# Performance work log

Measured on AMD Instinct MI355X. Metric: run time of the kernel, lower is better.

## Reference

```python
import jax, jax.numpy as jnp
import numpy as np

NUM_STUDENTS = 50000
NUM_PROBLEMS = 10000
EMBED_DIM = 64
NNZ = 3200000


def _spmm(rows, cols, vals, x, num_out):
    # out[r] = sum_{edges e with rows[e]==r} vals[e] * x[cols[e]]
    msgs = vals[:, None] * x[cols]  # [nnz, d]
    return jax.ops.segment_sum(msgs, rows, num_segments=num_out)


def setup_inputs() -> dict:
    key = jax.random.key(0)
    ks = jax.random.split(key, 8)
    return {
        "student_embeds": jax.random.normal(ks[0], (NUM_STUDENTS, EMBED_DIM), jnp.float32),
        "problem_embeds": jax.random.normal(ks[1], (NUM_PROBLEMS, EMBED_DIM), jnp.float32),
        "a_rows": jax.random.randint(ks[2], (NNZ,), 0, NUM_STUDENTS, jnp.int32),
        "a_cols": jax.random.randint(ks[3], (NNZ,), 0, NUM_PROBLEMS, jnp.int32),
        "a_vals": jax.random.uniform(ks[4], (NNZ,), jnp.float32),
        "ia_rows": jax.random.randint(ks[5], (NNZ,), 0, NUM_STUDENTS, jnp.int32),
        "ia_cols": jax.random.randint(ks[6], (NNZ,), 0, NUM_PROBLEMS, jnp.int32),
        "ia_vals": jax.random.uniform(ks[7], (NNZ,), jnp.float32),
    }


def reference(student_embeds, problem_embeds, a_rows, a_cols, a_vals,
              ia_rows, ia_cols, ia_vals):
    num_students = student_embeds.shape[0]
    num_problems = problem_embeds.shape[0]
    # a_matrix @ problem_embeds
    student_embeds_c = _spmm(a_rows, a_cols, a_vals, problem_embeds, num_students)
    # a_matrix.T @ student_embeds (swap roles of rows/cols)
    problem_embeds_c = _spmm(a_cols, a_rows, a_vals, student_embeds, num_problems)
    student_embeds_ic = _spmm(ia_rows, ia_cols, ia_vals, problem_embeds, num_students)
    problem_embeds_ic = _spmm(ia_cols, ia_rows, ia_vals, student_embeds, num_problems)
    return (student_embeds_c, student_embeds_ic, problem_embeds_c, problem_embeds_ic)
```

## Files before the change

### kernel.cpp

```cpp
#include <hip/hip_runtime.h>
#include <hip/hip_bf16.h>

#define NBMAX 256
#define TILE  4096
#define KPT   16
#define BINSMAX 512

__device__ __forceinline__ int seg8(unsigned r, unsigned mult8) {
    return (int)__umulhi(r, mult8);
}

__global__ __launch_bounds__(256) void hist_all(
        const int* __restrict__ k0, const int* __restrict__ k1,
        const int* __restrict__ k2, const int* __restrict__ k3,
        int* __restrict__ gcnt4, int nnz, int rsh_s, int rsh_p) {
    __shared__ int h[NBMAX];
    int dir = blockIdx.x & 3;
    const int* key = (dir == 0) ? k0 : (dir == 1) ? k1 : (dir == 2) ? k2 : k3;
    int rsh = (dir & 1) ? rsh_p : rsh_s;
    h[threadIdx.x] = 0;
    __syncthreads();
    int ch = blockIdx.x >> 2, nch = gridDim.x >> 2;
    int nnz4 = nnz >> 2;
    for (int i = ch * 256 + threadIdx.x; i < nnz4; i += nch * 256) {
        int4 k4 = ((const int4*)key)[i];
        atomicAdd(&h[k4.x >> rsh], 1);
        atomicAdd(&h[k4.y >> rsh], 1);
        atomicAdd(&h[k4.z >> rsh], 1);
        atomicAdd(&h[k4.w >> rsh], 1);
    }
    if (ch == 0) {
        for (int i = (nnz4 << 2) + threadIdx.x; i < nnz; i += 256)
            atomicAdd(&h[key[i] >> rsh], 1);
    }
    __syncthreads();
    int v = h[threadIdx.x];
    if (v) atomicAdd(&gcnt4[dir * NBMAX + threadIdx.x], v);
}

__global__ __launch_bounds__(256) void scan_all(
        const int* __restrict__ gcnt4, int* __restrict__ boffs4,
        int* __restrict__ bcur4, int nb_s, int nb_p, int nnz,
        int* __restrict__ offsE, int* __restrict__ offsO, int NS, int NP8) {
    __shared__ int tmp[NBMAX];
    int dir = blockIdx.x, tid = threadIdx.x;
    int nb = (dir & 1) ? nb_p : nb_s;
    int v = (tid < nb) ? gcnt4[dir * NBMAX + tid] : 0;
    tmp[tid] = v;
    __syncthreads();
    for (int off = 1; off < NBMAX; off <<= 1) {
        int t = (tid >= off) ? tmp[tid - off] : 0;
        __syncthreads();
        tmp[tid] += t;
        __syncthreads();
    }
    if (tid < nb) {
        int e = tmp[tid] - v;
        boffs4[dir * (NBMAX + 1) + tid] = e;
        bcur4[dir * NBMAX + tid] = e;
    }
    if (tid == 0) boffs4[dir * (NBMAX + 1) + nb] = nnz;
    if (dir == 0 && tid == 0) { offsE[NS] = nnz; offsO[NP8] = nnz; }
}

__global__ __launch_bounds__(256) void staged_scatter(
        const int* __restrict__ key, const int* __restrict__ other,
        const float* __restrict__ vals, int* __restrict__ cursor,
        uint2* __restrict__ edges, int nnz, int rsh) {
    __shared__ int lhist[NBMAX], lofs[NBMAX], lbase[NBMAX];
    __shared__ uint2 stage[TILE];
    __shared__ int   sslot[TILE];
    int tid = threadIdx.x;
    int lmask = (1 << rsh) - 1;
    int ntiles = (nnz + TILE - 1) / TILE;
    for (int tile = blockIdx.x; tile < ntiles; tile += gridDim.x) {
        int tbeg = tile * TILE;
        int n = nnz - tbeg; if (n > TILE) n = TILE;
        lhist[tid] = 0;
        __syncthreads();
        int myb[KPT], myr[KPT]; unsigned myo[KPT]; float myv[KPT];
        #pragma unroll
        for (int g = 0; g < 4; ++g) {
            int s = g * 1024 + tid * 4;
            if (s + 4 <= n) {
                int i = tbeg + s;
                int4   k4 = *(const int4*)(key + i);
                int4   o4 = *(const int4*)(other + i);
                float4 v4 = *(const float4*)(vals + i);
                int   kk[4] = {k4.x, k4.y, k4.z, k4.w};
                int   oo[4] = {o4.x, o4.y, o4.z, o4.w};
                float vv[4] = {v4.x, v4.y, v4.z, v4.w};
                #pragma unroll
                for (int k = 0; k < 4; ++k) {
                    int m = g * 4 + k;
                    myb[m] = kk[k] >> rsh;
                    myo[m] = (unsigned)oo[k] | ((unsigned)(kk[k] & lmask) << 16);
                    myv[m] = vv[k];
                    myr[m] = atomicAdd(&lhist[myb[m]], 1);
                }
            } else {
                #pragma unroll
                for (int k = 0; k < 4; ++k) {
                    int m = g * 4 + k;
                    int s2 = s + k;
                    if (s2 < n) {
                        int i = tbeg + s2;
                        int ky = key[i];
                        myb[m] = ky >> rsh;
                        myo[m] = (unsigned)other[i] | ((unsigned)(ky & lmask) << 16);
                        myv[m] = vals[i];
                        myr[m] = atomicAdd(&lhist[myb[m]], 1);
                    } else myb[m] = -1;
                }
            }
        }
        __syncthreads();
        int h = lhist[tid];
        lofs[tid] = h;
        __syncthreads();
        for (int off = 1; off < NBMAX; off <<= 1) {
            int t = (tid >= off) ? lofs[tid - off] : 0;
            __syncthreads();
            lofs[tid] += t;
            __syncthreads();
        }
        lofs[tid] -= h;
        if (h > 0) lbase[tid] = atomicAdd(&cursor[tid], h);
        __syncthreads();
        #pragma unroll
        for (int k = 0; k < KPT; ++k) {
            if (myb[k] >= 0) {
                int ls = lofs[myb[k]] + myr[k];
                stage[ls] = make_uint2(myo[k], __float_as_uint(myv[k]));
                sslot[ls] = lbase[myb[k]] + myr[k];
            }
        }
        __syncthreads();
        #pragma unroll
        for (int k = 0; k < KPT; ++k) {
            int s = k * 256 + tid;
            if (s < n) edges[sslot[s]] = stage[s];
        }
        __syncthreads();
    }
}

__global__ __launch_bounds__(512) void row_sort1(
        const uint2* __restrict__ e1, uint2* __restrict__ e2,
        const int* __restrict__ boffs, int* __restrict__ offs,
        int odd, int nb, int rsh, int nrows, unsigned mult8) {
    __shared__ int cnt[BINSMAX];
    __shared__ int tot[512];
    int tid = threadIdx.x;
    int b = blockIdx.x;
    if (b >= nb) return;
    int bins = odd ? (8 << rsh) : (1 << rsh);
    int beg = boffs[b], end = boffs[b + 1];
    if (tid < bins) cnt[tid] = 0;
    __syncthreads();
    for (int i = beg + tid; i < end; i += 512) {
        uint2 e = e1[i];
        int lrow = (int)(e.x >> 16);
        int bin = odd ? (lrow * 8 + seg8(e.x & 0xFFFFu, mult8)) : lrow;
        atomicAdd(&cnt[bin], 1);
    }
    __syncthreads();
    int own = (tid < bins) ? cnt[tid] : 0;
    tot[tid] = own;
    __syncthreads();
    for (int off = 1; off < 512; off <<= 1) {
        int t = (tid >= off) ? tot[tid - off] : 0;
        __syncthreads();
        tot[tid] += t;
        __syncthreads();
    }
    if (tid < bins) {
        int fineoff = tot[tid] - own;
        cnt[tid] = beg + fineoff;
        if (!odd) {
            int row = (b << rsh) + tid;
            if (row < nrows) offs[row] = beg + fineoff;
        } else {
            int row = (b << rsh) + (tid >> 3);
            if (row < nrows) offs[(row << 3) + (tid & 7)] = beg + fineoff;
        }
    }
    __syncthreads();
    for (int i = beg + tid; i < end; i += 512) {
        uint2 e = e1[i];
        int lrow = (int)(e.x >> 16);
        int bin = odd ? (lrow * 8 + seg8(e.x & 0xFFFFu, mult8)) : lrow;
        int slot = atomicAdd(&cnt[bin], 1);
        e2[slot] = make_uint2(e.x & 0xFFFFu, e.y);
    }
}

__device__ __forceinline__ void chunk_accum(
        float4& acc, uint2 e, int n, const float* __restrict__ xq, int q) {
    int   c0 = __shfl((int)e.x, q);
    float v0 = __uint_as_float(__shfl((int)e.y, q));
    int   c1 = __shfl((int)e.x, 4 + q);
    float v1 = __uint_as_float(__shfl((int)e.y, 4 + q));
    float4 x0 = *(const float4*)(xq + (((size_t)c0) << 6));
    float4 x1 = *(const float4*)(xq + (((size_t)c1) << 6));
    for (int j = 8; j < n; j += 8) {
        int   nc0 = __shfl((int)e.x, j + q);
        float nv0 = __uint_as_float(__shfl((int)e.y, j + q));
        int   nc1 = __shfl((int)e.x, j + 4 + q);
        float nv1 = __uint_as_float(__shfl((int)e.y, j + 4 + q));
        float4 nx0 = *(const float4*)(xq + (((size_t)nc0) << 6));
        float4 nx1 = *(const float4*)(xq + (((size_t)nc1) << 6));
        acc.x += v0 * x0.x; acc.y += v0 * x0.y;
        acc.z += v0 * x0.z; acc.w += v0 * x0.w;
        acc.x += v1 * x1.x; acc.y += v1 * x1.y;
        acc.z += v1 * x1.z; acc.w += v1 * x1.w;
        v0 = nv0; v1 = nv1; x0 = nx0; x1 = nx1;
    }
    acc.x += v0 * x0.x; acc.y += v0 * x0.y;
    acc.z += v0 * x0.z; acc.w += v0 * x0.w;
    acc.x += v1 * x1.x; acc.y += v1 * x1.y;
    acc.z += v1 * x1.z; acc.w += v1 * x1.w;
}

__device__ __forceinline__ float4 gather_pre(
        uint2 e0, int beg, int end, const uint2* __restrict__ edges,
        const float* __restrict__ xq, int q, int lane) {
    float4 acc = make_float4(0.f, 0.f, 0.f, 0.f);
    int n0 = end - beg; if (n0 > 64) n0 = 64;
    chunk_accum(acc, e0, n0, xq, q);
    for (int base = beg + 64; base < end; base += 64) {
        int n = end - base; if (n > 64) n = 64;
        uint2 e = make_uint2(0u, 0u);
        if (lane < n) e = edges[base + lane];
        chunk_accum(acc, e, n, xq, q);
    }
    acc.x += __shfl_xor(acc.x, 16); acc.y += __shfl_xor(acc.y, 16);
    acc.z += __shfl_xor(acc.z, 16); acc.w += __shfl_xor(acc.w, 16);
    acc.x += __shfl_xor(acc.x, 32); acc.y += __shfl_xor(acc.y, 32);
    acc.z += __shfl_xor(acc.z, 32); acc.w += __shfl_xor(acc.w, 32);
    return acc;
}

__global__ __launch_bounds__(256) void row_gather(
        const int* __restrict__ offs, const uint2* __restrict__ edges,
        const float* __restrict__ x, float* __restrict__ out, int nrows) {
    int wave = threadIdx.x >> 6, lane = threadIdx.x & 63;
    int q = lane >> 4, l16 = lane & 15;
    const float* xq = x + (l16 << 2);
    int rA = blockIdx.x * 8 + wave * 2;
    if (rA >= nrows) return;
    int rB = rA + 1;
    int begA = offs[rA], endA = offs[rA + 1];
    int begB = 0, endB = 0;
    if (rB < nrows) { begB = offs[rB]; endB = offs[rB + 1]; }
    int nA = endA - begA; if (nA > 64) nA = 64;
    int nB = endB - begB; if (nB > 64) nB = 64;
    uint2 eA = make_uint2(0u, 0u), eB = make_uint2(0u, 0u);
    if (lane < nA) eA = edges[begA + lane];
    if (lane < nB) eB = edges[begB + lane];
    float4 accA = gather_pre(eA, begA, endA, edges, xq, q, lane);
    if ((lane >> 4) == 0)
        *(float4*)(out + (((size_t)rA) << 6) + (l16 << 2)) = accA;
    if (rB < nrows) {
        float4 accB = gather_pre(eB, begB, endB, edges, xq, q, lane);
        if ((lane >> 4) == 0)
            *(float4*)(out + (((size_t)rB) << 6) + (l16 << 2)) = accB;
    }
}

__global__ __launch_bounds__(256) void xcd_gather(
        const int* __restrict__ offs, const uint2* __restrict__ edges,
        const float* __restrict__ x, float* __restrict__ partial, int NP) {
    int g = blockIdx.x;
    int slot = g & 7;
    int t = g >> 3;
    int wave = threadIdx.x >> 6, lane = threadIdx.x & 63;
    int q = lane >> 4, l16 = lane & 15;
    const float* xq = x + (l16 << 2);
    int rA = t * 8 + wave * 2;
    if (rA >= NP) return;
    int rB = rA + 1;
    int binA = rA * 8 + slot;
    int begA = offs[binA], endA = offs[binA + 1];
    int begB = 0, endB = 0;
    if (rB < NP) { int binB = rB * 8 + slot; begB = offs[binB]; endB = offs[binB + 1]; }
    int nA = endA - begA; if (nA > 64) nA = 64;
    int nB = endB - begB; if (nB > 64) nB = 64;
    uint2 eA = make_uint2(0u, 0u), eB = make_uint2(0u, 0u);
    if (lane < nA) eA = edges[begA + lane];
    if (lane < nB) eB = edges[begB + lane];
    float4 accA = gather_pre(eA, begA, endA, edges, xq, q, lane);
    if ((lane >> 4) == 0)
        *(float4*)(partial + (size_t)slot * NP * 64 + (((size_t)rA) << 6) + (l16 << 2)) = accA;
    if (rB < NP) {
        float4 accB = gather_pre(eB, begB, endB, edges, xq, q, lane);
        if ((lane >> 4) == 0)
            *(float4*)(partial + (size_t)slot * NP * 64 + (((size_t)rB) << 6) + (l16 << 2)) = accB;
    }
}

__global__ __launch_bounds__(256) void reduce8(
        const float* __restrict__ partial, float* __restrict__ out, int n4) {
    int i = blockIdx.x * 256 + threadIdx.x;
    if (i < n4) {
        const float4* p = (const float4*)partial;
        float4 s = make_float4(0.f, 0.f, 0.f, 0.f);
        #pragma unroll
        for (int xx = 0; xx < 8; ++xx) {
            float4 v = p[(size_t)xx * n4 + i];
            s.x += v.x; s.y += v.y; s.z += v.z; s.w += v.w;
        }
        ((float4*)out)[i] = s;
    }
}

__global__ void spmm_scatter_kernel(const int* __restrict__ rows, const int* __restrict__ cols,
                                    const float* __restrict__ vals,
                                    const float* __restrict__ s_emb, const float* __restrict__ p_emb,
                                    float* __restrict__ out_s, float* __restrict__ out_p, int nnz) {
    long long t = (long long)blockIdx.x * blockDim.x + threadIdx.x;
    int e = (int)(t >> 6);
    int d = (int)(t & 63);
    if (e >= nnz) return;
    int r = rows[e];
    int c = cols[e];
    float v = vals[e];
    atomicAdd(&out_s[(size_t)r * 64 + d], v * p_emb[(size_t)c * 64 + d]);
    atomicAdd(&out_p[(size_t)c * 64 + d], v * s_emb[(size_t)r * 64 + d]);
}

extern "C" void kernel_launch(void* const* d_in, const int* in_sizes, int n_in,
                              void* d_out, int out_size, void* d_ws, size_t ws_size,
                              hipStream_t stream) {
    const float* s_emb   = (const float*)d_in[0];
    const float* p_emb   = (const float*)d_in[1];
    const int*   a_rows  = (const int*)d_in[2];
    const int*   a_cols  = (const int*)d_in[3];
    const float* a_vals  = (const float*)d_in[4];
    const int*   ia_rows = (const int*)d_in[5];
    const int*   ia_cols = (const int*)d_in[6];
    const float* ia_vals = (const float*)d_in[7];

    const int NS  = in_sizes[0] / 64;
    const int NP  = in_sizes[1] / 64;
    const int nnz = in_sizes[2];
    const int NP8 = NP * 8;

    float* out = (float*)d_out;
    float* out_sc  = out;
    float* out_sic = out_sc  + (size_t)NS * 64;
    float* out_pc  = out_sic + (size_t)NS * 64;
    float* out_pic = out_pc  + (size_t)NP * 64;

    int rsh_s = 0; while ((((long long)NS + (1LL << rsh_s) - 1) >> rsh_s) > NBMAX) rsh_s++;
    int rsh_p = 0; while ((((long long)NP + (1LL << rsh_p) - 1) >> rsh_p) > NBMAX) rsh_p++;
    int nb_s = (NS + (1 << rsh_s) - 1) >> rsh_s;
    int nb_p = (NP + (1 << rsh_p) - 1) >> rsh_p;
    unsigned mult8 = (unsigned)((8ULL << 32) / (unsigned)NS);

    const size_t edges_bytes = (size_t)nnz * sizeof(uint2);
    const size_t offsE_bytes = (size_t)(NS + 1) * sizeof(int);
    const size_t offsO_bytes = (size_t)(NP8 + 1) * sizeof(int);
    const size_t need = 2 * edges_bytes + offsE_bytes + offsO_bytes
                      + (size_t)(4 * NBMAX + 4 * (NBMAX + 1) + 4 * NBMAX) * sizeof(int) + 256;
    const bool packable = (NS <= 0xFFFF) && (NP <= 0xFFFF) &&
                          ((1 << rsh_s) <= BINSMAX) && ((8 << rsh_p) <= BINSMAX) &&
                          (edges_bytes >= (size_t)NP8 * 64 * sizeof(float)) &&
                          ((NP * 64) % 4 == 0);

    if (ws_size < need || !packable) {
        hipMemsetAsync(d_out, 0, (size_t)out_size * sizeof(float), stream);
        const long long total = (long long)nnz * 64;
        const int grid = (int)((total + 255) / 256);
        spmm_scatter_kernel<<<grid, 256, 0, stream>>>(a_rows, a_cols, a_vals, s_emb, p_emb,
                                                      out_sc, out_pc, nnz);
        spmm_scatter_kernel<<<grid, 256, 0, stream>>>(ia_rows, ia_cols, ia_vals, s_emb, p_emb,
                                                      out_sic, out_pic, nnz);
        return;
    }

    char* w = (char*)d_ws;
    uint2* edges1 = (uint2*)w;  w += edges_bytes;
    uint2* edges2 = (uint2*)w;  w += edges_bytes;
    int*   offsE  = (int*)w;    w += offsE_bytes;
    int*   offsO  = (int*)w;    w += offsO_bytes;
    int*   gcnt4  = (int*)w;    w += 4 * NBMAX * sizeof(int);
    int*   boffs4 = (int*)w;    w += 4 * (NBMAX + 1) * sizeof(int);
    int*   bcur4  = (int*)w;
    float* partial = (float*)edges1;

    hipMemsetAsync(gcnt4, 0, 4 * NBMAX * sizeof(int), stream);
    hist_all<<<1024, 256, 0, stream>>>(a_rows, a_cols, ia_rows, ia_cols,
                                       gcnt4, nnz, rsh_s, rsh_p);
    scan_all<<<4, 256, 0, stream>>>(gcnt4, boffs4, bcur4, nb_s, nb_p, nnz,
                                    offsE, offsO, NS, NP8);

    const int ntiles = (nnz + TILE - 1) / TILE;

    struct Dir { const int* key; const int* other; const float* vals;
                 float* out; int odd; };
    Dir dirs[4] = {
        { a_rows,  a_cols,  a_vals,  out_sc,  0 },
        { a_cols,  a_rows,  a_vals,  out_pc,  1 },
        { ia_rows, ia_cols, ia_vals, out_sic, 0 },
        { ia_cols, ia_rows, ia_vals, out_pic, 1 },
    };
    for (int t = 0; t < 4; ++t) {
        const Dir& D = dirs[t];
        if (!D.odd) {
            staged_scatter<<<ntiles, 256, 0, stream>>>(D.key, D.other, D.vals,
                                                       bcur4 + t * NBMAX, edges1, nnz, rsh_s);
            row_sort1<<<nb_s, 512, 0, stream>>>(edges1, edges2,
                                                boffs4 + t * (NBMAX + 1), offsE,
                                                0, nb_s, rsh_s, NS, mult8);
            row_gather<<<(NS + 7) / 8, 256, 0, stream>>>(offsE, edges2, p_emb, D.out, NS);
        } else {
            staged_scatter<<<ntiles, 256, 0, stream>>>(D.key, D.other, D.vals,
                                                       bcur4 + t * NBMAX, edges1, nnz, rsh_p);
            row_sort1<<<nb_p, 512, 0, stream>>>(edges1, edges2,
                                                boffs4 + t * (NBMAX + 1), offsO,
                                                1, nb_p, rsh_p, NP, mult8);
            xcd_gather<<<8 * ((NP + 7) / 8), 256, 0, stream>>>(offsO, edges2,
                                                               s_emb, partial, NP);
            reduce8<<<(NP * 64 / 4 + 255) / 256, 256, 0, stream>>>(partial, D.out, NP * 64 / 4);
        }
    }
}
```

Baseline: 579.3 us.

## Fuse forward and transpose edge scatter into one pass per matrix

Adds a staged_scatter2 kernel that reads each matrix's rows, cols and vals once and bucket-scatters edges into two buffers, one keyed by student and one by problem. This replaces the two separate scatter passes per matrix, cutting input reads and kernel launches roughly in half for the scatter phase. It needs a third edge-sized workspace buffer, uses smaller tiles with double the shared-memory staging, and falls back to the old path when the workspace is too small.

```diff
diff --git a/kernel.cpp b/kernel.cpp
--- a/kernel.cpp
+++ b/kernel.cpp
@@ -4,6 +4,8 @@
 #define NBMAX 256
 #define TILE  4096
 #define KPT   16
+#define FTILE 2048
+#define FKPT  8
 #define BINSMAX 512
 
 __device__ __forceinline__ int seg8(unsigned r, unsigned mult8) {
@@ -145,6 +147,107 @@
     }
 }
 
+__global__ __launch_bounds__(256) void staged_scatter2(
+        const int* __restrict__ krow, const int* __restrict__ kcol,
+        const float* __restrict__ vals,
+        int* __restrict__ curE, int* __restrict__ curO,
+        uint2* __restrict__ edgesE, uint2* __restrict__ edgesO,
+        int nnz, int rsh_e, int rsh_o) {
+    __shared__ int lhistE[NBMAX], lofsE[NBMAX], lbaseE[NBMAX];
+    __shared__ int lhistO[NBMAX], lofsO[NBMAX], lbaseO[NBMAX];
+    __shared__ uint2 stageE[FTILE], stageO[FTILE];
+    __shared__ int   sslotE[FTILE], sslotO[FTILE];
+    int tid = threadIdx.x;
+    int lmE = (1 << rsh_e) - 1, lmO = (1 << rsh_o) - 1;
+    int ntiles = (nnz + FTILE - 1) / FTILE;
+    for (int tile = blockIdx.x; tile < ntiles; tile += gridDim.x) {
+        int tbeg = tile * FTILE;
+        int n = nnz - tbeg; if (n > FTILE) n = FTILE;
+        lhistE[tid] = 0; lhistO[tid] = 0;
+        __syncthreads();
+        int mbE[FKPT], mrE[FKPT]; unsigned moE[FKPT];
+        int mbO[FKPT], mrO[FKPT]; unsigned moO[FKPT];
+        float mv[FKPT];
+        #pragma unroll
+        for (int g = 0; g < 2; ++g) {
+            int s = g * 1024 + tid * 4;
+            if (s + 4 <= n) {
+                int i = tbeg + s;
+                int4   r4 = *(const int4*)(krow + i);
+                int4   c4 = *(const int4*)(kcol + i);
+                float4 v4 = *(const float4*)(vals + i);
+                int   rr[4] = {r4.x, r4.y, r4.z, r4.w};
+                int   cc[4] = {c4.x, c4.y, c4.z, c4.w};
+                float vv[4] = {v4.x, v4.y, v4.z, v4.w};
+                #pragma unroll
+                for (int k = 0; k < 4; ++k) {
+                    int m = g * 4 + k;
+                    mv[m]  = vv[k];
+                    mbE[m] = rr[k] >> rsh_e;
+                    moE[m] = (unsigned)cc[k] | ((unsigned)(rr[k] & lmE) << 16);
+                    mrE[m] = atomicAdd(&lhistE[mbE[m]], 1);
+                    mbO[m] = cc[k] >> rsh_o;
+                    moO[m] = (unsigned)rr[k] | ((unsigned)(cc[k] & lmO) << 16);
+                    mrO[m] = atomicAdd(&lhistO[mbO[m]], 1);
+                }
+            } else {
+                #pragma unroll
+                for (int k = 0; k < 4; ++k) {
+                    int m = g * 4 + k;
+                    int s2 = s + k;
+                    if (s2 < n) {
+                        int i = tbeg + s2;
+                        int r = krow[i], c = kcol[i];
+                        mv[m]  = vals[i];
+                        mbE[m] = r >> rsh_e;
+                        moE[m] = (unsigned)c | ((unsigned)(r & lmE) << 16);
+                        mrE[m] = atomicAdd(&lhistE[mbE[m]], 1);
+                        mbO[m] = c >> rsh_o;
+                        moO[m] = (unsigned)r | ((unsigned)(c & lmO) << 16);
+                        mrO[m] = atomicAdd(&lhistO[mbO[m]], 1);
+                    } else { mbE[m] = -1; mbO[m] = -1; }
+                }
+            }
+        }
+        __syncthreads();
+        int hE = lhistE[tid], hO = lhistO[tid];
+        lofsE[tid] = hE; lofsO[tid] = hO;
+        __syncthreads();
+        for (int off = 1; off < NBMAX; off <<= 1) {
+            int tE = (tid >= off) ? lofsE[tid - off] : 0;
+            int tO = (tid >= off) ? lofsO[tid - off] : 0;
+            __syncthreads();
+            lofsE[tid] += tE; lofsO[tid] += tO;
+            __syncthreads();
+        }
+        lofsE[tid] -= hE; lofsO[tid] -= hO;
+        if (hE > 0) lbaseE[tid] = atomicAdd(&curE[tid], hE);
+        if (hO > 0) lbaseO[tid] = atomicAdd(&curO[tid], hO);
+        __syncthreads();
+        #pragma unroll
+        for (int k = 0; k < FKPT; ++k) {
+            if (mbE[k] >= 0) {
+                int lsE = lofsE[mbE[k]] + mrE[k];
+                stageE[lsE] = make_uint2(moE[k], __float_as_uint(mv[k]));
+                sslotE[lsE] = lbaseE[mbE[k]] + mrE[k];
+                int lsO = lofsO[mbO[k]] + mrO[k];
+                stageO[lsO] = make_uint2(moO[k], __float_as_uint(mv[k]));
+                sslotO[lsO] = lbaseO[mbO[k]] + mrO[k];
+            }
+        }
+        __syncthreads();
+        #pragma unroll
+        for (int k = 0; k < FKPT; ++k) {
+            int s = k * 256 + tid;
+            if (s < n) {
+                edgesE[sslotE[s]] = stageE[s];
+                edgesO[sslotO[s]] = stageO[s];
+            }
+        }
+        __syncthreads();
+    }
+}
+
 __global__ __launch_bounds__(512) void row_sort1(
         const uint2* __restrict__ e1, uint2* __restrict__ e2,
         const int* __restrict__ boffs, int* __restrict__ offs,
@@ -361,8 +464,10 @@
     const size_t edges_bytes = (size_t)nnz * sizeof(uint2);
     const size_t offsE_bytes = (size_t)(NS + 1) * sizeof(int);
     const size_t offsO_bytes = (size_t)(NP8 + 1) * sizeof(int);
-    const size_t need = 2 * edges_bytes + offsE_bytes + offsO_bytes
+    const size_t fixed_bytes = offsE_bytes + offsO_bytes
                       + (size_t)(4 * NBMAX + 4 * (NBMAX + 1) + 4 * NBMAX) * sizeof(int) + 256;
+    const size_t need  = 2 * edges_bytes + fixed_bytes;
+    const size_t need3 = 3 * edges_bytes + fixed_bytes;
     const bool packable = (NS <= 0xFFFF) && (NP <= 0xFFFF) &&
                           ((1 << rsh_s) <= BINSMAX) && ((8 << rsh_p) <= BINSMAX) &&
                           (edges_bytes >= (size_t)NP8 * 64 * sizeof(float)) &&
@@ -379,15 +484,18 @@
         return;
     }
 
+    const bool fused = (ws_size >= need3);
+
     char* w = (char*)d_ws;
     uint2* edges1 = (uint2*)w;  w += edges_bytes;
     uint2* edges2 = (uint2*)w;  w += edges_bytes;
+    uint2* edges3 = nullptr;
+    if (fused) { edges3 = (uint2*)w; w += edges_bytes; }
     int*   offsE  = (int*)w;    w += offsE_bytes;
     int*   offsO  = (int*)w;    w += offsO_bytes;
     int*   gcnt4  = (int*)w;    w += 4 * NBMAX * sizeof(int);
     int*   boffs4 = (int*)w;    w += 4 * (NBMAX + 1) * sizeof(int);
     int*   bcur4  = (int*)w;
-    float* partial = (float*)edges1;
 
     hipMemsetAsync(gcnt4, 0, 4 * NBMAX * sizeof(int), stream);
     hist_all<<<1024, 256, 0, stream>>>(a_rows, a_cols, ia_rows, ia_cols,
@@ -395,8 +503,34 @@
     scan_all<<<4, 256, 0, stream>>>(gcnt4, boffs4, bcur4, nb_s, nb_p, nnz,
                                     offsE, offsO, NS, NP8);
 
+    if (fused) {
+        const int ntiles2 = (nnz + FTILE - 1) / FTILE;
+        struct Mat { const int* r; const int* c; const float* v;
+                     float* oe; float* oo; int de, dodd; };
+        Mat mats[2] = {
+            { a_rows,  a_cols,  a_vals,  out_sc,  out_pc,  0, 1 },
+            { ia_rows, ia_cols, ia_vals, out_sic, out_pic, 2, 3 },
+        };
+        for (int m = 0; m < 2; ++m) {
+            const Mat& M = mats[m];
+            staged_scatter2<<<ntiles2, 256, 0, stream>>>(M.r, M.c, M.v,
+                    bcur4 + M.de * NBMAX, bcur4 + M.dodd * NBMAX,
+                    edges1, edges3, nnz, rsh_s, rsh_p);
+            row_sort1<<<nb_s, 512, 0, stream>>>(edges1, edges2,
+                    boffs4 + M.de * (NBMAX + 1), offsE, 0, nb_s, rsh_s, NS, mult8);
+            row_gather<<<(NS + 7) / 8, 256, 0, stream>>>(offsE, edges2, p_emb, M.oe, NS);
+            row_sort1<<<nb_p, 512, 0, stream>>>(edges3, edges1,
+                    boffs4 + M.dodd * (NBMAX + 1), offsO, 1, nb_p, rsh_p, NP, mult8);
+            xcd_gather<<<8 * ((NP + 7) / 8), 256, 0, stream>>>(offsO, edges1,
+                    s_emb, (float*)edges3, NP);
+            reduce8<<<(NP * 64 / 4 + 255) / 256, 256, 0, stream>>>((float*)edges3,
+                    M.oo, NP * 64 / 4);
+        }
+        return;
+    }
+
+    float* partial = (float*)edges1;
     const int ntiles = (nnz + TILE - 1) / TILE;
-
     struct Dir { const int* key; const int* other; const float* vals;
                  float* out; int odd; };
     Dir dirs[4] = {
```

New measurement: 558.0 us. 1.04x faster.
